# Performance work log

Measured on AMD Instinct MI355X. Metric: run time of the kernel, lower is better.

The kernel has to match this reference:

```python
import jax, jax.numpy as jnp
import numpy as np

H, W = 260, 346          # DAVIS346 sensor resolution
TEMP = 256.0             # time-decay temperature
B, T = 16, 4096          # batch, event sequence length
C = 2 * H + 2 * W        # pred channel dim = 1212


def setup_inputs() -> dict:
    key = jax.random.key(0)
    k1, k2, k3, k4, k5 = jax.random.split(key, 5)
    pred = jax.random.normal(k1, (B, T, C), dtype=jnp.float32)
    # target columns: [timestamp, y_index, x_index, polarity]
    t = jnp.sort(jax.random.uniform(k2, (B, T), minval=0.0, maxval=1.0e6), axis=1)
    y = jax.random.randint(k3, (B, T), 0, H)
    x = jax.random.randint(k4, (B, T), 0, W)
    p = jax.random.randint(k5, (B, T), 0, 2)
    target = jnp.stack([t,
                        y.astype(jnp.float32),
                        x.astype(jnp.float32),
                        p.astype(jnp.float32)], axis=-1)  # [B,T,4]
    return {"pred": pred, "target": target}


def _loss(pred, target):
    t = target[..., 0]                          # [B,T] timestamps
    y = target[..., 1].astype(jnp.int32)        # row indices
    x = target[..., 2].astype(jnp.int32)        # col indices
    p = target[..., 3]                          # polarity in {0,1}
    p_ = p[..., None]

    oh_y = jax.nn.one_hot(y, H, dtype=pred.dtype)   # [B,T,H]
    oh_x = jax.nn.one_hot(x, W, dtype=pred.dtype)   # [B,T,W]
    # scatter targets, concatenated in pred's channel layout [H0|H1|W0|W1]
    base = jnp.concatenate([oh_y * (1.0 - p_), oh_y * p_,
                            oh_x * (1.0 - p_), oh_x * p_], axis=-1)  # [B,T,C]

    # exponential time decay between consecutive events: d_i = exp(-(t_{i+1}-t_i)/TEMP)
    decay = jnp.exp(-(t[:, 1:] - t[:, :-1]) / TEMP)  # [B,T-1]

    # reverse recurrence: s_{T-1} = base_{T-1}; s_i = base_i + d_i * s_{i+1} for i = T-2..1;
    # s_0 = base_0 (torch loop stops before updating index 0)
    base_tm = jnp.swapaxes(base, 0, 1)               # [T,B,C] time-major
    decay_tm = jnp.swapaxes(decay, 0, 1)[..., None]  # [T-1,B,1]

    def step(carry, xd):
        b, d = xd
        s = b + d * carry
        return s, s

    _, ys = jax.lax.scan(step, base_tm[-1], (base_tm[:-1], decay_tm), reverse=True)
    s = jnp.concatenate([ys, base_tm[-1:]], axis=0)  # [T,B,C]
    s = s.at[0].set(base_tm[0])                      # index 0 never accumulated
    s = jnp.swapaxes(s, 0, 1)                        # [B,T,C]

    segs = [(0, H), (H, 2 * H), (2 * H, 2 * H + W), (2 * H + W, C)]
    losses = []
    for a, b in segs:
        logp = jax.nn.log_softmax(pred[..., a:b], axis=-1)
        soft = jax.nn.softmax(s[..., a:b], axis=-1)
        losses.append(-(soft * logp).sum(-1))        # soft-target CE, [B,T]
    lH0, lH1, lW0, lW1 = losses

    loss = ((lH0 + lW0) * (1.0 - p) + (lH1 + lW1) * p).mean()
    return loss


def reference(pred, target):
    return _loss(pred, target)
```

## Files before the change

### kernel.cpp

```cpp
#include <hip/hip_runtime.h>

#define HH 260
#define WW 346
#define CC 1212
#define CP 1280
#define HALF 640
#define NA 606
#define BB 16
#define TT 4096
#define INV_TEMP (1.0f/256.0f)
#define KCH 256
#define LCH 16
#define NG 16
#define GSZ 16
#define GLEN (GSZ * LCH)

__global__ __launch_bounds__(256) void p12_scan(const float* __restrict__ target,
                                                float* __restrict__ LCin,
                                                float* __restrict__ GroupL) {
    const int blk = blockIdx.x;
    const int sl = blk % 5;
    const int bg = blk / 5;
    const int b = bg >> 4, g = bg & 15;
    const int tid = threadIdx.x;
    const int c = sl * 256 + tid;
    const int a0 = g * GLEN;

    __shared__ float tg[GLEN][4];
    __shared__ float tnextS;
    for (int idx = tid; idx < GLEN * 4; idx += 256)
        tg[idx >> 2][idx & 3] = target[((size_t)b * TT + a0) * 4 + idx];
    if (tid == 0) tnextS = (a0 + GLEN < TT) ? target[((size_t)b * TT + a0 + GLEN) * 4] : 0.0f;
    __syncthreads();

    float carry = 0.f;
    for (int k = GSZ - 1; k >= 0; --k) {
        LCin[((size_t)(b * KCH + g * GSZ + k)) * CP + c] = carry;
#pragma unroll
        for (int q = LCH - 1; q >= 0; --q) {
            const int li = k * LCH + q;
            const int i = a0 + li;
            const float ti = tg[li][0];
            const float tn = (li == GLEN - 1) ? tnextS : tg[li + 1][0];
            const float d = (i >= TT - 1) ? 0.f : __expf(-(tn - ti) * INV_TEMP);
            const int y = (int)tg[li][1], x = (int)tg[li][2], p = (int)tg[li][3];
            const int cy = p * HALF + y;
            const int cx = p * HALF + 260 + x;
            const float add = ((c == cy) ? 1.f : 0.f) + ((c == cx) ? 1.f : 0.f);
            carry = fmaf(carry, d, add);
        }
    }
    GroupL[(size_t)bg * CP + c] = carry;
}

__global__ __launch_bounds__(256) void p2b(const float* __restrict__ target,
                                           const float* __restrict__ GroupL,
                                           float* __restrict__ SC) {
    const int blk = blockIdx.x;
    const int ct = blk % 5;
    const int b = blk / 5;
    const int c = ct * 256 + threadIdx.x;

    float Gv[NG], GP[NG];
#pragma unroll
    for (int g = 0; g < NG; ++g)
        Gv[g] = GroupL[((size_t)(b * NG + g)) * CP + c];
#pragma unroll
    for (int g = 0; g < NG; ++g) {
        if (g < NG - 1) {
            const float ta = target[((size_t)b * TT + g * GLEN) * 4];
            const float te = target[((size_t)b * TT + (g + 1) * GLEN) * 4];
            GP[g] = __expf(-(te - ta) * INV_TEMP);
        } else GP[g] = 0.f;
    }
    float carry = 0.f;
#pragma unroll
    for (int g = NG - 1; g >= 0; --g) {
        SC[((size_t)(b * NG + g)) * CP + c] = carry;
        carry = fmaf(GP[g], carry, Gv[g]);
    }
}

__global__ __launch_bounds__(256, 4) void p3_loss(const float* __restrict__ pred,
                                                  const float* __restrict__ target,
                                                  const float* __restrict__ LCin,
                                                  const float* __restrict__ SC,
                                                  double* __restrict__ partials) {
    const int blk = blockIdx.x;
    const int b = blk >> 6;
    const int k0 = (blk & 63) << 2;
    const int tid = threadIdx.x;
    const int w = tid >> 6, lane = tid & 63;
    const int k = k0 + w;
    const int g = k >> 4;
    const int a = k * LCH;

    __shared__ float tg[4][LCH][4];
    __shared__ float tnextS[4];
    tg[tid >> 6][(tid >> 2) & 15][tid & 3] =
        target[((size_t)b * TT + k0 * LCH) * 4 + tid];
    if (tid < 4) {
        const int kk = k0 + tid;
        tnextS[tid] = (kk < KCH - 1) ? target[((size_t)b * TT + (kk + 1) * LCH) * 4] : 0.0f;
    }
    __syncthreads();

    float Qk = 0.f;
    if (g < NG - 1) {
        const float tge = target[((size_t)b * TT + (g + 1) * GLEN) * 4];
        const float tk1 = target[((size_t)b * TT + (k + 1) * LCH) * 4];
        Qk = __expf(-(tge - tk1) * INV_TEMP);
    }

    const float* __restrict__ lc = LCin + (size_t)(b * KCH + k) * CP;
    const float* __restrict__ sc = SC + ((size_t)(b * NG + g)) * CP;
    float s0[10], s1[10];
#pragma unroll
    for (int q = 0; q < 5; ++q) {
        const int u0 = (q * 64 + lane) * 2;
        const float2 l0 = *(const float2*)(lc + u0);
        const float2 c0 = *(const float2*)(sc + u0);
        const float2 l1 = *(const float2*)(lc + HALF + u0);
        const float2 c1 = *(const float2*)(sc + HALF + u0);
        s0[2 * q]     = fmaf(Qk, c0.x, l0.x);
        s0[2 * q + 1] = fmaf(Qk, c0.y, l0.y);
        s1[2 * q]     = fmaf(Qk, c1.x, l1.x);
        s1[2 * q + 1] = fmaf(Qk, c1.y, l1.y);
    }

    auto loadRow = [&](float (&pr)[10], int li) {
        const int pn = (int)tg[w][li][3];
        const float* __restrict__ prow = pred + ((size_t)b * TT + a + li) * CC;
#pragma unroll
        for (int q = 0; q < 5; ++q) {
            const int u0 = (q * 64 + lane) * 2;
            float2 v;
            if (u0 < 260) {
                v = *(const float2*)(prow + pn * HH + u0);
            } else if (u0 < NA) {
                v = *(const float2*)(prow + 2 * HH + pn * WW + (u0 - 260));
            } else {
                v = make_float2(0.f, 0.f);
            }
            pr[2 * q] = v.x; pr[2 * q + 1] = v.y;
        }
    };

    double lacc = 0.0;

    auto step = [&](int li, float (&pr)[10]) {
        const int i = a + li;
        const float ti = tg[w][li][0];
        const float tn = (li == LCH - 1) ? tnextS[w] : tg[w][li + 1][0];
        const float d = (i == 0 || i >= TT - 1) ? 0.0f : __expf(-(tn - ti) * INV_TEMP);
        const int y = (int)tg[w][li][1], x = (int)tg[w][li][2], p = (int)tg[w][li][3];
        const int uy = y, ux = 260 + x;

        float zpy = 0.f, zsy = 0.f, dty = 0.f;
        float zpx = 0.f, zsx = 0.f, dtx = 0.f;

        auto inner = [&](float (&SA)[10], float (&SO)[10]) {
#pragma unroll
            for (int q = 0; q < 5; ++q) {
#pragma unroll
                for (int e = 0; e < 2; ++e) {
                    const int j = 2 * q + e;
                    const int u = (q * 64 + lane) * 2 + e;
                    const float add = ((u == uy) ? 1.f : 0.f) + ((u == ux) ? 1.f : 0.f);
                    SA[j] = fmaf(SA[j], d, add);
                    SO[j] *= d;
                    float es = __expf(SA[j]);
                    float ep = __expf(pr[j]);
                    if (q == 4) {
                        const float m = (u < NA) ? 1.f : 0.f;
                        es *= m; ep *= m;
                    }
                    if (u < 260) {
                        zpy += ep; zsy += es; dty = fmaf(es, pr[j], dty);
                    } else {
                        zpx += ep; zsx += es; dtx = fmaf(es, pr[j], dtx);
                    }
                }
            }
        };
        if (p == 0) inner(s0, s1); else inner(s1, s0);

#pragma unroll
        for (int off = 32; off > 0; off >>= 1) {
            zpy += __shfl_xor(zpy, off);
            zsy += __shfl_xor(zsy, off);
            dty += __shfl_xor(dty, off);
            zpx += __shfl_xor(zpx, off);
            zsx += __shfl_xor(zsx, off);
            dtx += __shfl_xor(dtx, off);
        }
        const float loss = __logf(zpy) + __logf(zpx)
                         - __fdividef(dty, zsy) - __fdividef(dtx, zsx);
        lacc += (double)loss;
    };

    float prA[10], prB[10];
    loadRow(prA, LCH - 1);
    loadRow(prB, LCH - 2);
    for (int t = 0; t < LCH / 2; ++t) {
        const int liA = LCH - 1 - 2 * t;
        step(liA, prA);
        if (liA - 2 >= 0) loadRow(prA, liA - 2);
        const int liB = LCH - 2 - 2 * t;
        step(liB, prB);
        if (liB - 2 >= 0) loadRow(prB, liB - 2);
    }

    if (lane == 0) partials[b * KCH + k] = lacc;
}

__global__ void p4_final(const double* __restrict__ partials, float* __restrict__ out) {
    const int tid = threadIdx.x;
    double sum = 0.0;
    for (int i = tid; i < BB * KCH; i += 256) sum += partials[i];
#pragma unroll
    for (int off = 32; off > 0; off >>= 1) sum += __shfl_xor(sum, off);
    __shared__ double sred[4];
    if ((tid & 63) == 0) sred[tid >> 6] = sum;
    __syncthreads();
    if (tid == 0)
        out[0] = (float)((sred[0] + sred[1] + sred[2] + sred[3]) / (double)((size_t)BB * TT));
}

extern "C" void kernel_launch(void* const* d_in, const int* in_sizes, int n_in,
                              void* d_out, int out_size, void* d_ws, size_t ws_size,
                              hipStream_t stream) {
    const float* pred   = (const float*)d_in[0];
    const float* target = (const float*)d_in[1];
    float* out = (float*)d_out;

    double* partials = (double*)d_ws;
    float* LCin   = (float*)((char*)d_ws + 65536);
    float* GroupL = LCin + (size_t)BB * KCH * CP;
    float* SC     = GroupL + (size_t)BB * NG * CP;

    p12_scan<<<BB * NG * 5, 256, 0, stream>>>(target, LCin, GroupL);
    p2b<<<BB * 5, 256, 0, stream>>>(target, GroupL, SC);
    p3_loss<<<BB * KCH / 4, 256, 0, stream>>>(pred, target, LCin, SC, partials);
    p4_final<<<1, 256, 0, stream>>>(partials, out);
}
```

Before: 96.51 us.

## Fuse group-carry and final reduction into preceding kernels via last-block atomic counters

Removes two kernel launches. The per-batch group-carry scan now runs inside p12_scan in whichever block is last to finish for that batch, detected through an atomic counter. The final sum of partials runs in the last p3_loss block the same way, and a memset resets the counters on each call. The p3 channel layout also changes from strided float2 loads to scalar loads with stride 64, and the two-row software pipeline becomes a single prefetch-next-row loop. The tradeoff is a serialized tail in the last block plus one extra memset, and scalar loads may use memory less efficiently.

```diff
diff --git a/kernel.cpp b/kernel.cpp
--- a/kernel.cpp
+++ b/kernel.cpp
@@ -14,10 +14,13 @@
 #define NG 16
 #define GSZ 16
 #define GLEN (GSZ * LCH)
+#define NJ 10
 
 __global__ __launch_bounds__(256) void p12_scan(const float* __restrict__ target,
                                                 float* __restrict__ LCin,
-                                                float* __restrict__ GroupL) {
+                                                float* __restrict__ GroupL,
+                                                float* __restrict__ SC,
+                                                int* __restrict__ ctr) {
     const int blk = blockIdx.x;
     const int sl = blk % 5;
     const int bg = blk / 5;
@@ -28,6 +31,7 @@
 
     __shared__ float tg[GLEN][4];
     __shared__ float tnextS;
+    __shared__ int lastS;
     for (int idx = tid; idx < GLEN * 4; idx += 256)
         tg[idx >> 2][idx & 3] = target[((size_t)b * TT + a0) * 4 + idx];
     if (tid == 0) tnextS = (a0 + GLEN < TT) ? target[((size_t)b * TT + a0 + GLEN) * 4] : 0.0f;
@@ -51,33 +55,34 @@
         }
     }
     GroupL[(size_t)bg * CP + c] = carry;
-}
-
-__global__ __launch_bounds__(256) void p2b(const float* __restrict__ target,
-                                           const float* __restrict__ GroupL,
-                                           float* __restrict__ SC) {
-    const int blk = blockIdx.x;
-    const int ct = blk % 5;
-    const int b = blk / 5;
-    const int c = ct * 256 + threadIdx.x;
-
-    float Gv[NG], GP[NG];
-#pragma unroll
-    for (int g = 0; g < NG; ++g)
-        Gv[g] = GroupL[((size_t)(b * NG + g)) * CP + c];
-#pragma unroll
-    for (int g = 0; g < NG; ++g) {
-        if (g < NG - 1) {
-            const float ta = target[((size_t)b * TT + g * GLEN) * 4];
-            const float te = target[((size_t)b * TT + (g + 1) * GLEN) * 4];
-            GP[g] = __expf(-(te - ta) * INV_TEMP);
-        } else GP[g] = 0.f;
-    }
-    float carry = 0.f;
-#pragma unroll
-    for (int g = NG - 1; g >= 0; --g) {
-        SC[((size_t)(b * NG + g)) * CP + c] = carry;
-        carry = fmaf(GP[g], carry, Gv[g]);
+
+    __syncthreads();
+    if (tid == 0) {
+        __threadfence();
+        lastS = (atomicAdd(&ctr[b], 1) == NG * 5 - 1) ? 1 : 0;
+    }
+    __syncthreads();
+    if (lastS) {
+        __threadfence();
+        for (int it = 0; it < 5; ++it) {
+            const int cc = it * 256 + tid;
+            float Gv[NG];
+#pragma unroll
+            for (int gg = 0; gg < NG; ++gg)
+                Gv[gg] = GroupL[((size_t)(b * NG + gg)) * CP + cc];
+            float c2 = 0.f;
+#pragma unroll
+            for (int gg = NG - 1; gg >= 0; --gg) {
+                SC[((size_t)(b * NG + gg)) * CP + cc] = c2;
+                float GP = 0.f;
+                if (gg < NG - 1) {
+                    const float ta = target[((size_t)b * TT + gg * GLEN) * 4];
+                    const float te = target[((size_t)b * TT + (gg + 1) * GLEN) * 4];
+                    GP = __expf(-(te - ta) * INV_TEMP);
+                }
+                c2 = fmaf(GP, c2, Gv[gg]);
+            }
+        }
     }
 }
 
@@ -85,7 +90,9 @@
                                                   const float* __restrict__ target,
                                                   const float* __restrict__ LCin,
                                                   const float* __restrict__ SC,
-                                                  double* __restrict__ partials) {
+                                                  double* __restrict__ partials,
+                                                  float* __restrict__ out,
+                                                  int* __restrict__ ctr) {
     const int blk = blockIdx.x;
     const int b = blk >> 6;
     const int k0 = (blk & 63) << 2;
@@ -97,6 +104,8 @@
 
     __shared__ float tg[4][LCH][4];
     __shared__ float tnextS[4];
+    __shared__ int lastS;
+    __shared__ double sred[4];
     tg[tid >> 6][(tid >> 2) & 15][tid & 3] =
         target[((size_t)b * TT + k0 * LCH) * 4 + tid];
     if (tid < 4) {
@@ -114,41 +123,39 @@
 
     const float* __restrict__ lc = LCin + (size_t)(b * KCH + k) * CP;
     const float* __restrict__ sc = SC + ((size_t)(b * NG + g)) * CP;
-    float s0[10], s1[10];
-#pragma unroll
-    for (int q = 0; q < 5; ++q) {
-        const int u0 = (q * 64 + lane) * 2;
-        const float2 l0 = *(const float2*)(lc + u0);
-        const float2 c0 = *(const float2*)(sc + u0);
-        const float2 l1 = *(const float2*)(lc + HALF + u0);
-        const float2 c1 = *(const float2*)(sc + HALF + u0);
-        s0[2 * q]     = fmaf(Qk, c0.x, l0.x);
-        s0[2 * q + 1] = fmaf(Qk, c0.y, l0.y);
-        s1[2 * q]     = fmaf(Qk, c1.x, l1.x);
-        s1[2 * q + 1] = fmaf(Qk, c1.y, l1.y);
-    }
-
-    auto loadRow = [&](float (&pr)[10], int li) {
-        const int pn = (int)tg[w][li][3];
-        const float* __restrict__ prow = pred + ((size_t)b * TT + a + li) * CC;
-#pragma unroll
-        for (int q = 0; q < 5; ++q) {
-            const int u0 = (q * 64 + lane) * 2;
-            float2 v;
-            if (u0 < 260) {
-                v = *(const float2*)(prow + pn * HH + u0);
-            } else if (u0 < NA) {
-                v = *(const float2*)(prow + 2 * HH + pn * WW + (u0 - 260));
-            } else {
-                v = make_float2(0.f, 0.f);
+    float s0[NJ], s1[NJ];
+#pragma unroll
+    for (int j = 0; j < NJ; ++j) {
+        const int u = lane + 64 * j;
+        s0[j] = fmaf(Qk, sc[u], lc[u]);
+        s1[j] = fmaf(Qk, sc[HALF + u], lc[HALF + u]);
+    }
+
+    float prA[NJ], prB[NJ];
+    {
+        const int p = (int)tg[w][LCH - 1][3];
+        const float* __restrict__ prow = pred + ((size_t)b * TT + a + LCH - 1) * CC;
+#pragma unroll
+        for (int j = 0; j < NJ; ++j) {
+            const int u = lane + 64 * j;
+            const int c = (u < 260) ? p * HH + u : 2 * HH + p * WW + (u - 260);
+            prA[j] = (u < NA) ? prow[c] : 0.0f;
+        }
+    }
+
+    double lacc = 0.0;
+    for (int li = LCH - 1; li >= 0; --li) {
+        if (li > 0) {
+            const int pn = (int)tg[w][li - 1][3];
+            const float* __restrict__ prow = pred + ((size_t)b * TT + a + li - 1) * CC;
+#pragma unroll
+            for (int j = 0; j < NJ; ++j) {
+                const int u = lane + 64 * j;
+                const int c = (u < 260) ? pn * HH + u : 2 * HH + pn * WW + (u - 260);
+                prB[j] = (u < NA) ? prow[c] : 0.0f;
             }
-            pr[2 * q] = v.x; pr[2 * q + 1] = v.y;
-        }
-    };
-
-    double lacc = 0.0;
-
-    auto step = [&](int li, float (&pr)[10]) {
+        }
+
         const int i = a + li;
         const float ti = tg[w][li][0];
         const float tn = (li == LCH - 1) ? tnextS[w] : tg[w][li + 1][0];
@@ -159,27 +166,31 @@
         float zpy = 0.f, zsy = 0.f, dty = 0.f;
         float zpx = 0.f, zsx = 0.f, dtx = 0.f;
 
-        auto inner = [&](float (&SA)[10], float (&SO)[10]) {
-#pragma unroll
-            for (int q = 0; q < 5; ++q) {
-#pragma unroll
-                for (int e = 0; e < 2; ++e) {
-                    const int j = 2 * q + e;
-                    const int u = (q * 64 + lane) * 2 + e;
-                    const float add = ((u == uy) ? 1.f : 0.f) + ((u == ux) ? 1.f : 0.f);
-                    SA[j] = fmaf(SA[j], d, add);
-                    SO[j] *= d;
-                    float es = __expf(SA[j]);
-                    float ep = __expf(pr[j]);
-                    if (q == 4) {
-                        const float m = (u < NA) ? 1.f : 0.f;
-                        es *= m; ep *= m;
-                    }
-                    if (u < 260) {
-                        zpy += ep; zsy += es; dty = fmaf(es, pr[j], dty);
-                    } else {
-                        zpx += ep; zsx += es; dtx = fmaf(es, pr[j], dtx);
-                    }
+        auto inner = [&](float (&SA)[NJ], float (&SO)[NJ]) {
+#pragma unroll
+            for (int j = 0; j < NJ; ++j) {
+                const int u = lane + 64 * j;
+                const float add = (u == uy ? 1.f : 0.f) + (u == ux ? 1.f : 0.f);
+                SA[j] = fmaf(SA[j], d, add);
+                SO[j] *= d;
+                float es = __expf(SA[j]);
+                float ep = __expf(prA[j]);
+                if (j == NJ - 1) {
+                    const float m = (u < NA) ? 1.f : 0.f;
+                    es *= m; ep *= m;
+                }
+                if (j < 4) {
+                    zpy += ep; zsy += es; dty = fmaf(es, prA[j], dty);
+                } else if (j == 4) {
+                    const bool isY = (u < 260);
+                    zpy += isY ? ep : 0.f;
+                    zsy += isY ? es : 0.f;
+                    dty = fmaf(isY ? es : 0.f, prA[j], dty);
+                    zpx += isY ? 0.f : ep;
+                    zsx += isY ? 0.f : es;
+                    dtx = fmaf(isY ? 0.f : es, prA[j], dtx);
+                } else {
+                    zpx += ep; zsx += es; dtx = fmaf(es, prA[j], dtx);
                 }
             }
         };
@@ -197,34 +208,29 @@
         const float loss = __logf(zpy) + __logf(zpx)
                          - __fdividef(dty, zsy) - __fdividef(dtx, zsx);
         lacc += (double)loss;
-    };
-
-    float prA[10], prB[10];
-    loadRow(prA, LCH - 1);
-    loadRow(prB, LCH - 2);
-    for (int t = 0; t < LCH / 2; ++t) {
-        const int liA = LCH - 1 - 2 * t;
-        step(liA, prA);
-        if (liA - 2 >= 0) loadRow(prA, liA - 2);
-        const int liB = LCH - 2 - 2 * t;
-        step(liB, prB);
-        if (liB - 2 >= 0) loadRow(prB, liB - 2);
-    }
-
+
+#pragma unroll
+        for (int j = 0; j < NJ; ++j) prA[j] = prB[j];
+    }
     if (lane == 0) partials[b * KCH + k] = lacc;
-}
-
-__global__ void p4_final(const double* __restrict__ partials, float* __restrict__ out) {
-    const int tid = threadIdx.x;
-    double sum = 0.0;
-    for (int i = tid; i < BB * KCH; i += 256) sum += partials[i];
-#pragma unroll
-    for (int off = 32; off > 0; off >>= 1) sum += __shfl_xor(sum, off);
-    __shared__ double sred[4];
-    if ((tid & 63) == 0) sred[tid >> 6] = sum;
-    __syncthreads();
-    if (tid == 0)
-        out[0] = (float)((sred[0] + sred[1] + sred[2] + sred[3]) / (double)((size_t)BB * TT));
+
+    __syncthreads();
+    if (tid == 0) {
+        __threadfence();
+        lastS = (atomicAdd(&ctr[16], 1) == (int)gridDim.x - 1) ? 1 : 0;
+    }
+    __syncthreads();
+    if (lastS) {
+        __threadfence();
+        double sum = 0.0;
+        for (int i2 = tid; i2 < BB * KCH; i2 += 256) sum += partials[i2];
+#pragma unroll
+        for (int off = 32; off > 0; off >>= 1) sum += __shfl_xor(sum, off);
+        if ((tid & 63) == 0) sred[tid >> 6] = sum;
+        __syncthreads();
+        if (tid == 0)
+            out[0] = (float)((sred[0] + sred[1] + sred[2] + sred[3]) / (double)((size_t)BB * TT));
+    }
 }
 
 extern "C" void kernel_launch(void* const* d_in, const int* in_sizes, int n_in,
@@ -235,12 +241,12 @@
     float* out = (float*)d_out;
 
     double* partials = (double*)d_ws;
+    int* ctr = (int*)((char*)d_ws + 32768);
     float* LCin   = (float*)((char*)d_ws + 65536);
     float* GroupL = LCin + (size_t)BB * KCH * CP;
     float* SC     = GroupL + (size_t)BB * NG * CP;
 
-    p12_scan<<<BB * NG * 5, 256, 0, stream>>>(target, LCin, GroupL);
-    p2b<<<BB * 5, 256, 0, stream>>>(target, GroupL, SC);
-    p3_loss<<<BB * KCH / 4, 256, 0, stream>>>(pred, target, LCin, SC, partials);
-    p4_final<<<1, 256, 0, stream>>>(partials, out);
+    hipMemsetAsync(ctr, 0, 32 * sizeof(int), stream);
+    p12_scan<<<BB * NG * 5, 256, 0, stream>>>(target, LCin, GroupL, SC, ctr);
+    p3_loss<<<BB * KCH / 4, 256, 0, stream>>>(pred, target, LCin, SC, partials, out, ctr);
 }
```

After: 151.8 us. 57.2% more time.
